# Performance work log

Hardware: AMD Instinct MI355X
Metric: run time of the kernel (lower is better)

## Reference

```python
import jax, jax.numpy as jnp
import numpy as np

N, D, E = 50000, 128, 600000
EPS = 1e-5  # LayerNorm eps (torch default)


def setup_inputs() -> dict:
    key = jax.random.key(0)
    ks = jax.random.split(key, 8)
    s = D ** -0.5
    return {
        "in_feat": jax.random.normal(ks[0], (N, D), dtype=jnp.float32),
        "edge_src": jax.random.randint(ks[1], (E,), 0, N),
        "edge_dst": jax.random.randint(ks[2], (E,), 0, N),
        "W1": jax.random.normal(ks[3], (D, D), dtype=jnp.float32) * s,
        "b1": jnp.zeros((D,), jnp.float32),
        "W2": jax.random.normal(ks[4], (D, D), dtype=jnp.float32) * s,
        "b2": jnp.zeros((D,), jnp.float32),
        "ln1_w": jnp.ones((D,), jnp.float32),
        "ln1_b": jnp.zeros((D,), jnp.float32),
        "ln2_w": jnp.ones((D,), jnp.float32),
        "ln2_b": jnp.zeros((D,), jnp.float32),
    }


def layer_norm(x, w, b):
    mu = jnp.mean(x, axis=-1, keepdims=True)
    var = jnp.var(x, axis=-1, keepdims=True)
    return (x - mu) * jax.lax.rsqrt(var + EPS) * w + b


def gcn_conv(x, W, b, src, dst, deg_inv_sqrt):
    # PyG GCNConv: linear transform, then D^-1/2 (A+I) D^-1/2 propagation, then bias
    h = x @ W  # [N, D]
    norm = deg_inv_sqrt[src] * deg_inv_sqrt[dst]  # [E]
    agg = jax.ops.segment_sum(h[src] * norm[:, None], dst, num_segments=N)
    agg = agg + (deg_inv_sqrt ** 2)[:, None] * h  # self-loop term handled analytically
    return agg + b


def reference(in_feat, W1, b1, W2, b2, ln1_w, ln1_b, ln2_w, ln2_b, edge_src, edge_dst):
    # degree with self-loops, computed on destination (PyG convention)
    deg = jax.ops.segment_sum(jnp.ones((E,), in_feat.dtype), edge_dst, num_segments=N) + 1.0
    dis = jax.lax.rsqrt(deg)
    h = gcn_conv(in_feat, W1, b1, edge_src, edge_dst, dis)
    ori = in_feat  # in_feats == h_feats -> residual uses original input
    ln_params = [(ln1_w, ln1_b), (ln2_w, ln2_b)]
    for i in range(2):  # prop_step - 1 iterations
        h = h + ori  # res=True, residual=1.0
        h = layer_norm(h, *ln_params[i])
        h = jax.nn.relu(h)  # dropout=0 -> identity
        h = gcn_conv(h, W2, b2, edge_src, edge_dst, dis)
    return h
```

## Files before the change

### kernel.cpp

```cpp
#include <hip/hip_runtime.h>
#include <hip/hip_bf16.h>

typedef unsigned short bf16_t;
typedef __attribute__((ext_vector_type(4))) float f32x4;
typedef __attribute__((ext_vector_type(8))) unsigned short us8;

#define CAP 64

__device__ __forceinline__ float bf2f(bf16_t u) {
  return __uint_as_float(((unsigned int)u) << 16);
}
__device__ __forceinline__ bf16_t f2bf(float f) {
  unsigned int u = __float_as_uint(f);
  return (bf16_t)((u + 0x7FFFu + ((u >> 16) & 1u)) >> 16);
}
__device__ __forceinline__ void acc2(float2& a, unsigned int d) {
  a.x += __uint_as_float(d << 16);
  a.y += __uint_as_float(d & 0xffff0000u);
}

__global__ void UnifiedGNN_56521769616171_kernel() {}


__global__ void gnn_zero(int* cnt, int n, bf16_t* Azrow, bf16_t* A2zrow,
                         const float* W1, const float* W2,
                         bf16_t* Wt1g, bf16_t* Wt2g) {
  int gid = blockIdx.x * 256 + threadIdx.x;
  if (blockIdx.x == 0 && threadIdx.x < 64) {
    ((unsigned int*)Azrow)[threadIdx.x] = 0u;
    ((unsigned int*)A2zrow)[threadIdx.x] = 0u;
  }
  if (gid < 4096) {
    const float* W = (gid < 2048) ? W1 : W2;
    bf16_t* dst = (gid < 2048) ? Wt1g : Wt2g;
    int j = gid & 2047;
    int c = j & 127;
    int kb = j >> 7;
    int k0 = kb << 3;
    us8 v;
#pragma unroll
    for (int q = 0; q < 8; q++) v[q] = f2bf(W[(size_t)(k0 + q) * 128 + c]);
    ((us8*)dst)[c * 16 + (kb ^ (c & 15))] = v;
  }
  if (gid < n) cnt[gid] = 0;
}

__global__ void gnn_fill(const int* src, const int* dst, int* cnt,
                         int* csr, int e, int n) {
  int i = blockIdx.x * 256 + threadIdx.x;
  if (i < e) {
    int d = dst[i];
    if (d >= 0 && d < n) {
      int pos = atomicAdd(&cnt[d], 1);
      if (pos < CAP) csr[(size_t)d * CAP + pos] = src[i];
    }
  }
}

__global__ __launch_bounds__(512) void gnn_gemm(const void* Xv,
    const bf16_t* Wg, const int* cnt, bf16_t* A, int n, int xfmt) {
  __shared__ __align__(16) bf16_t Wt[128 * 128];
  int tid = threadIdx.x;

  for (int j = tid; j < 2048; j += 512)
    ((us8*)Wt)[j] = ((const us8*)Wg)[j];
  __syncthreads();

  int lane = tid & 63;
  int wid = tid >> 6;
  int l15 = lane & 15;
  int lk = lane >> 4;
  const bf16_t* Xb = (const bf16_t*)Xv;
  const float* Xf = (const float*)Xv;

  int rowbase = blockIdx.x * 128 + wid * 16;
  int arow = rowbase + l15;
  int arc = arow < n ? arow : (n - 1);

  f32x4 acc[8];
#pragma unroll
  for (int c = 0; c < 8; c++) {
    acc[c][0] = 0.0f; acc[c][1] = 0.0f; acc[c][2] = 0.0f; acc[c][3] = 0.0f;
  }

#pragma unroll
  for (int ks = 0; ks < 4; ks++) {
    int kb = ks * 4 + lk;
    us8 ah, al;
    if (xfmt == 0) {
      float4 a0 = *(const float4*)(Xf + (size_t)arc * 128 + kb * 8);
      float4 a1 = *(const float4*)(Xf + (size_t)arc * 128 + kb * 8 + 4);
      ah[0] = f2bf(a0.x); al[0] = f2bf(a0.x - bf2f(ah[0]));
      ah[1] = f2bf(a0.y); al[1] = f2bf(a0.y - bf2f(ah[1]));
      ah[2] = f2bf(a0.z); al[2] = f2bf(a0.z - bf2f(ah[2]));
      ah[3] = f2bf(a0.w); al[3] = f2bf(a0.w - bf2f(ah[3]));
      ah[4] = f2bf(a1.x); al[4] = f2bf(a1.x - bf2f(ah[4]));
      ah[5] = f2bf(a1.y); al[5] = f2bf(a1.y - bf2f(ah[5]));
      ah[6] = f2bf(a1.z); al[6] = f2bf(a1.z - bf2f(ah[6]));
      ah[7] = f2bf(a1.w); al[7] = f2bf(a1.w - bf2f(ah[7]));
    } else {
      ah = *(const us8*)(Xb + (size_t)arc * 128 + kb * 8);
    }
#pragma unroll
    for (int c = 0; c < 8; c++) {
      int col = c * 16 + l15;
      us8 bf = *(const us8*)&Wt[col * 128 + ((kb ^ l15) << 3)];
      asm volatile("s_nop 2\n\tv_mfma_f32_16x16x32_bf16 %0, %1, %2, %0"
                   : "+v"(acc[c]) : "v"(ah), "v"(bf));
    }
    if (xfmt == 0) {
#pragma unroll
      for (int c = 0; c < 8; c++) {
        int col = c * 16 + l15;
        us8 bf = *(const us8*)&Wt[col * 128 + ((kb ^ l15) << 3)];
        asm volatile("s_nop 2\n\tv_mfma_f32_16x16x32_bf16 %0, %1, %2, %0"
                     : "+v"(acc[c]) : "v"(al), "v"(bf));
      }
    }
  }
  asm volatile("s_nop 7\n\ts_nop 7"
               : "+v"(acc[0]), "+v"(acc[1]), "+v"(acc[2]), "+v"(acc[3]),
                 "+v"(acc[4]), "+v"(acc[5]), "+v"(acc[6]), "+v"(acc[7]));

#pragma unroll
  for (int j = 0; j < 4; j++) {
    int row = rowbase + lk * 4 + j;
    if (row < n) {
      float dd = rsqrtf((float)cnt[row] + 1.0f);
#pragma unroll
      for (int c = 0; c < 8; c++) {
        A[(size_t)row * 128 + c * 16 + l15] = f2bf(acc[c][j] * dd);
      }
    }
  }
}

__global__ __launch_bounds__(512) void gnn_agg_gemm(const bf16_t* Ain,
    const int* cnt, const int* csr, const float* bias, const float* ori,
    const float* lnw, const float* lnb, const bf16_t* Wg,
    bf16_t* Aout, int n) {
  __shared__ __align__(16) bf16_t Wt[128 * 128];
  __shared__ __align__(16) bf16_t Bs[128 * 128];
  int tid = threadIdx.x;
  int lane = tid & 63;
  int wid = tid >> 6;
  int g = lane >> 4;
  int l16 = lane & 15;

  for (int j = tid; j < 2048; j += 512)
    ((us8*)Wt)[j] = ((const us8*)Wg)[j];

  const uint4* Av4 = (const uint4*)Ain;

  for (int rr = 0; rr < 4; rr++) {
    int rt = wid * 16 + rr * 4 + g;
    int row = blockIdx.x * 128 + rt;
    int rc = row < n ? row : (n - 1);
    int c = cnt[rc];
    int pc = (c + 15) & ~15;
    if (pc > CAP) pc = CAP;
    const int* crow = csr + (size_t)rc * CAP;

    float2 ac[4];
#pragma unroll
    for (int i = 0; i < 4; i++) ac[i] = make_float2(0.0f, 0.0f);

    for (int e = 0; e < pc; e += 16) {
      int raw = crow[e + l16];
      int sv = (e + l16 < c) ? raw : n;
#pragma unroll
      for (int half = 0; half < 2; half++) {
        uint4 va[8];
#pragma unroll
        for (int j = 0; j < 8; j++) {
          int s = __shfl(sv, (g << 4) + half * 8 + j);
          va[j] = Av4[(size_t)s * 16 + l16];
        }
#pragma unroll
        for (int j = 0; j < 8; j++) {
          acc2(ac[0], va[j].x);
          acc2(ac[1], va[j].y);
          acc2(ac[2], va[j].z);
          acc2(ac[3], va[j].w);
        }
      }
    }
    {
      uint4 sv4 = Av4[(size_t)rc * 16 + l16];
      acc2(ac[0], sv4.x);
      acc2(ac[1], sv4.y);
      acc2(ac[2], sv4.z);
      acc2(ac[3], sv4.w);
    }

    float dd = rsqrtf((float)c + 1.0f);
    float4 bb0 = *(const float4*)(bias + l16 * 8);
    float4 bb1 = *(const float4*)(bias + l16 * 8 + 4);
    float4 o0 = *(const float4*)(ori + (size_t)rc * 128 + l16 * 8);
    float4 o1 = *(const float4*)(ori + (size_t)rc * 128 + l16 * 8 + 4);
    float v[8];
    v[0] = dd * ac[0].x + bb0.x + o0.x; v[1] = dd * ac[0].y + bb0.y + o0.y;
    v[2] = dd * ac[1].x + bb0.z + o0.z; v[3] = dd * ac[1].y + bb0.w + o0.w;
    v[4] = dd * ac[2].x + bb1.x + o1.x; v[5] = dd * ac[2].y + bb1.y + o1.y;
    v[6] = dd * ac[3].x + bb1.z + o1.z; v[7] = dd * ac[3].y + bb1.w + o1.w;
    float s = 0.0f, sq = 0.0f;
#pragma unroll
    for (int i = 0; i < 8; i++) { s += v[i]; sq += v[i] * v[i]; }
    for (int off = 8; off >= 1; off >>= 1) {
      s += __shfl_xor(s, off);
      sq += __shfl_xor(sq, off);
    }
    float mu = s * (1.0f / 128.0f);
    float var = sq * (1.0f / 128.0f) - mu * mu;
    float inv = rsqrtf(var + 1e-5f);
    float4 w0 = *(const float4*)(lnw + l16 * 8);
    float4 w1 = *(const float4*)(lnw + l16 * 8 + 4);
    float4 c0 = *(const float4*)(lnb + l16 * 8);
    float4 c1 = *(const float4*)(lnb + l16 * 8 + 4);
    float wv[8] = {w0.x, w0.y, w0.z, w0.w, w1.x, w1.y, w1.z, w1.w};
    float cv[8] = {c0.x, c0.y, c0.z, c0.w, c1.x, c1.y, c1.z, c1.w};
    us8 o8;
#pragma unroll
    for (int i = 0; i < 8; i++) {
      float y = (v[i] - mu) * inv * wv[i] + cv[i];
      if (y < 0.0f) y = 0.0f;
      o8[i] = f2bf(y);
    }
    *(us8*)&Bs[rt * 128 + ((l16 ^ (rt & 15)) << 3)] = o8;
  }

  __syncthreads();

  int l15 = lane & 15;
  int lk = lane >> 4;
  int rowbase = blockIdx.x * 128 + wid * 16;
  int rt0 = wid * 16 + l15;

  f32x4 acc[8];
#pragma unroll
  for (int c = 0; c < 8; c++) {
    acc[c][0] = 0.0f; acc[c][1] = 0.0f; acc[c][2] = 0.0f; acc[c][3] = 0.0f;
  }

#pragma unroll
  for (int ks = 0; ks < 4; ks++) {
    int kb = ks * 4 + lk;
    us8 ah = *(const us8*)&Bs[rt0 * 128 + ((kb ^ l15) << 3)];
#pragma unroll
    for (int c = 0; c < 8; c++) {
      int col = c * 16 + l15;
      us8 bf = *(const us8*)&Wt[col * 128 + ((kb ^ l15) << 3)];
      asm volatile("s_nop 2\n\tv_mfma_f32_16x16x32_bf16 %0, %1, %2, %0"
                   : "+v"(acc[c]) : "v"(ah), "v"(bf));
    }
  }
  asm volatile("s_nop 7\n\ts_nop 7"
               : "+v"(acc[0]), "+v"(acc[1]), "+v"(acc[2]), "+v"(acc[3]),
                 "+v"(acc[4]), "+v"(acc[5]), "+v"(acc[6]), "+v"(acc[7]));

#pragma unroll
  for (int j = 0; j < 4; j++) {
    int row = rowbase + lk * 4 + j;
    if (row < n) {
      float dd = rsqrtf((float)cnt[row] + 1.0f);
#pragma unroll
      for (int c = 0; c < 8; c++) {
        Aout[(size_t)row * 128 + c * 16 + l15] = f2bf(acc[c][j] * dd);
      }
    }
  }
}

__global__ void gnn_aggln(const bf16_t* A,
    const int* cnt, const int* csr, const float* bias,
    float* Fout, int n) {
  int wid = threadIdx.x >> 6;
  int lane = threadIdx.x & 63;
  int g = lane >> 4;
  int l16 = lane & 15;
  int row = blockIdx.x * 16 + wid * 4 + g;
  bool active = row < n;
  int rc = active ? row : (n - 1);
  int c = cnt[rc];
  int pc = (c + 15) & ~15;
  if (pc > CAP) pc = CAP;
  const int* crow = csr + (size_t)rc * CAP;
  const uint4* Av4 = (const uint4*)A;

  float2 ac[4];
#pragma unroll
  for (int i = 0; i < 4; i++) ac[i] = make_float2(0.0f, 0.0f);

  for (int e = 0; e < pc; e += 16) {
    int raw = crow[e + l16];
    int sv = (e + l16 < c) ? raw : n;
#pragma unroll
    for (int half = 0; half < 2; half++) {
      uint4 va[8];
#pragma unroll
      for (int j = 0; j < 8; j++) {
        int s = __shfl(sv, (g << 4) + half * 8 + j);
        va[j] = Av4[(size_t)s * 16 + l16];
      }
#pragma unroll
      for (int j = 0; j < 8; j++) {
        acc2(ac[0], va[j].x);
        acc2(ac[1], va[j].y);
        acc2(ac[2], va[j].z);
        acc2(ac[3], va[j].w);
      }
    }
  }
  {
    uint4 sv4 = Av4[(size_t)rc * 16 + l16];
    acc2(ac[0], sv4.x);
    acc2(ac[1], sv4.y);
    acc2(ac[2], sv4.z);
    acc2(ac[3], sv4.w);
  }

  float dd = rsqrtf((float)c + 1.0f);
  float4 bb0 = *(const float4*)(bias + l16 * 8);
  float4 bb1 = *(const float4*)(bias + l16 * 8 + 4);
  if (active) {
    float4 f0 = make_float4(dd * ac[0].x + bb0.x, dd * ac[0].y + bb0.y,
                            dd * ac[1].x + bb0.z, dd * ac[1].y + bb0.w);
    float4 f1 = make_float4(dd * ac[2].x + bb1.x, dd * ac[2].y + bb1.y,
                            dd * ac[3].x + bb1.z, dd * ac[3].y + bb1.w);
    *(float4*)(Fout + (size_t)rc * 128 + l16 * 8) = f0;
    *(float4*)(Fout + (size_t)rc * 128 + l16 * 8 + 4) = f1;
  }
}


extern "C" void kernel_launch(void* const* d_in, const int* in_sizes, int n_in,
                              void* d_out, int out_size, void* d_ws, size_t ws_size,
                              hipStream_t stream) {
  UnifiedGNN_56521769616171_kernel<<<1, 64, 0, stream>>>();

  int nI = (n_in > 0 && n_in <= 16) ? n_in : 11;
  long best = -1;
  int iFeat = 0;
  for (int i = 0; i < nI; i++)
    if ((long)in_sizes[i] > best) { best = in_sizes[i]; iFeat = i; }
  int iW[2], iV[6], iE[2];
  int nW = 0, nV = 0, nE = 0;
  for (int i = 0; i < nI; i++) {
    if (i == iFeat) continue;
    int s = in_sizes[i];
    if (s == 128 * 128) { if (nW < 2) iW[nW++] = i; }
    else if (s == 128)  { if (nV < 6) iV[nV++] = i; }
    else                { if (nE < 2) iE[nE++] = i; }
  }
  int aFeat = 0, aEs = 1, aEd = 2, aW1 = 3, aB1 = 4, aW2 = 5, aB2 = 6,
      aL1w = 7, aL1b = 8, aL2w = 9, aL2b = 10;
  if (nW == 2 && nV == 6 && nE == 2) {
    aFeat = iFeat;
    aEs = iE[0]; aEd = iE[1];
    aW1 = iW[0]; aW2 = iW[1];
    aB1 = iV[0]; aB2 = iV[1];
    aL1w = iV[2]; aL1b = iV[3]; aL2w = iV[4]; aL2b = iV[5];
  }

  int N = 50000;
  int E = 600000;
  if (in_sizes[aFeat] > 0 && (in_sizes[aFeat] % 128) == 0) N = in_sizes[aFeat] / 128;
  if (in_sizes[aEs] > 0) E = in_sizes[aEs];

  const float* in_feat = (const float*)d_in[aFeat];
  const int*   esrc    = (const int*)d_in[aEs];
  const int*   edst    = (const int*)d_in[aEd];
  const float* W1      = (const float*)d_in[aW1];
  const float* b1      = (const float*)d_in[aB1];
  const float* W2      = (const float*)d_in[aW2];
  const float* b2      = (const float*)d_in[aB2];
  const float* ln1w    = (const float*)d_in[aL1w];
  const float* ln1b    = (const float*)d_in[aL1b];
  const float* ln2w    = (const float*)d_in[aL2w];
  const float* ln2b    = (const float*)d_in[aL2b];

  char* base = (char*)d_ws;
  size_t off = 0;
  int* cnt = (int*)(base + off);      off += ((size_t)N * 4 + 255) & ~(size_t)255;
  int* csr = (int*)(base + off);      off += ((size_t)N * CAP * 4 + 255) & ~(size_t)255;
  bf16_t* A = (bf16_t*)(base + off);  off += ((size_t)(N + 1) * 256 + 255) & ~(size_t)255;
  bf16_t* A2 = (bf16_t*)(base + off); off += ((size_t)(N + 1) * 256 + 255) & ~(size_t)255;
  bf16_t* Wt1g = (bf16_t*)(base + off); off += 32768;
  bf16_t* Wt2g = (bf16_t*)(base + off); off += 32768;

  int gZ = (N + 255) / 256;
  int gE = (E + 255) / 256;
  int nt128 = (N + 127) / 128;
  int agg_grid = (N + 15) / 16;

  gnn_zero<<<gZ, 256, 0, stream>>>(cnt, N, A + (size_t)N * 128,
                                   A2 + (size_t)N * 128, W1, W2, Wt1g, Wt2g);
  gnn_fill<<<gE, 256, 0, stream>>>(esrc, edst, cnt, csr, E, N);

  gnn_gemm<<<nt128, 512, 0, stream>>>(in_feat, Wt1g, cnt, A, N, 0);

  gnn_agg_gemm<<<nt128, 512, 0, stream>>>(A, cnt, csr, b1, in_feat,
                                          ln1w, ln1b, Wt2g, A2, N);

  gnn_agg_gemm<<<nt128, 512, 0, stream>>>(A2, cnt, csr, b2, in_feat,
                                          ln2w, ln2b, Wt2g, A, N);

  gnn_aggln<<<agg_grid, 256, 0, stream>>>(A, cnt, csr, b2, (float*)d_out, N);
}
```

Before: 248.4 us.

## Fuse all GNN stages into one cooperative persistent kernel with grid syncs

```diff
diff --git a/kernel.cpp b/kernel.cpp
--- a/kernel.cpp
+++ b/kernel.cpp
@@ -1,5 +1,8 @@
 #include <hip/hip_runtime.h>
 #include <hip/hip_bf16.h>
+#include <hip/hip_cooperative_groups.h>
+
+namespace cg = cooperative_groups;
 
 typedef unsigned short bf16_t;
 typedef __attribute__((ext_vector_type(4))) float f32x4;
@@ -20,6 +23,313 @@
 }
 
 __global__ void UnifiedGNN_56521769616171_kernel() {}
+
+__device__ __forceinline__ void gather_row(const uint4* Av4, const int* crow,
+    int c, int pc, int nzero, int g, int l16, float2* ac) {
+  for (int e = 0; e < pc; e += 16) {
+    int raw = crow[e + l16];
+    int sv = (e + l16 < c) ? raw : nzero;
+#pragma unroll
+    for (int half = 0; half < 2; half++) {
+      uint4 va[8];
+#pragma unroll
+      for (int j = 0; j < 8; j++) {
+        int s = __shfl(sv, (g << 4) + half * 8 + j);
+        va[j] = Av4[(size_t)s * 16 + l16];
+      }
+#pragma unroll
+      for (int j = 0; j < 8; j++) {
+        acc2(ac[0], va[j].x);
+        acc2(ac[1], va[j].y);
+        acc2(ac[2], va[j].z);
+        acc2(ac[3], va[j].w);
+      }
+    }
+  }
+}
+
+__device__ __forceinline__ void agg_gemm_tile(const bf16_t* Ain, bf16_t* Aout,
+    const int* cnt, const int* csr, const float* bias, const float* ori,
+    const float* lnw, const float* lnb, bf16_t* Wt, bf16_t* Bs,
+    int n, int nt, int bid, int nblk) {
+  int tid = threadIdx.x;
+  int lane = tid & 63;
+  int wid = tid >> 6;
+  int g = lane >> 4;
+  int l16 = lane & 15;
+  const uint4* Av4 = (const uint4*)Ain;
+
+  for (int t = bid; t < nt; t += nblk) {
+    for (int rr = 0; rr < 4; rr++) {
+      int rt = wid * 16 + rr * 4 + g;
+      int row = t * 128 + rt;
+      int rc = row < n ? row : (n - 1);
+      int c = cnt[rc];
+      int pc = (c + 15) & ~15;
+      if (pc > CAP) pc = CAP;
+      float2 ac[4];
+#pragma unroll
+      for (int i = 0; i < 4; i++) ac[i] = make_float2(0.0f, 0.0f);
+      gather_row(Av4, csr + (size_t)rc * CAP, c, pc, n, g, l16, ac);
+      {
+        uint4 sv4 = Av4[(size_t)rc * 16 + l16];
+        acc2(ac[0], sv4.x);
+        acc2(ac[1], sv4.y);
+        acc2(ac[2], sv4.z);
+        acc2(ac[3], sv4.w);
+      }
+      float dd = rsqrtf((float)c + 1.0f);
+      float4 bb0 = *(const float4*)(bias + l16 * 8);
+      float4 bb1 = *(const float4*)(bias + l16 * 8 + 4);
+      float4 o0 = *(const float4*)(ori + (size_t)rc * 128 + l16 * 8);
+      float4 o1 = *(const float4*)(ori + (size_t)rc * 128 + l16 * 8 + 4);
+      float v[8];
+      v[0] = dd * ac[0].x + bb0.x + o0.x; v[1] = dd * ac[0].y + bb0.y + o0.y;
+      v[2] = dd * ac[1].x + bb0.z + o0.z; v[3] = dd * ac[1].y + bb0.w + o0.w;
+      v[4] = dd * ac[2].x + bb1.x + o1.x; v[5] = dd * ac[2].y + bb1.y + o1.y;
+      v[6] = dd * ac[3].x + bb1.z + o1.z; v[7] = dd * ac[3].y + bb1.w + o1.w;
+      float s = 0.0f, sq = 0.0f;
+#pragma unroll
+      for (int i = 0; i < 8; i++) { s += v[i]; sq += v[i] * v[i]; }
+      for (int off = 8; off >= 1; off >>= 1) {
+        s += __shfl_xor(s, off);
+        sq += __shfl_xor(sq, off);
+      }
+      float mu = s * (1.0f / 128.0f);
+      float var = sq * (1.0f / 128.0f) - mu * mu;
+      float inv = rsqrtf(var + 1e-5f);
+      float4 w0 = *(const float4*)(lnw + l16 * 8);
+      float4 w1 = *(const float4*)(lnw + l16 * 8 + 4);
+      float4 c0 = *(const float4*)(lnb + l16 * 8);
+      float4 c1 = *(const float4*)(lnb + l16 * 8 + 4);
+      float wv[8] = {w0.x, w0.y, w0.z, w0.w, w1.x, w1.y, w1.z, w1.w};
+      float cv[8] = {c0.x, c0.y, c0.z, c0.w, c1.x, c1.y, c1.z, c1.w};
+      us8 o8;
+#pragma unroll
+      for (int i = 0; i < 8; i++) {
+        float y = (v[i] - mu) * inv * wv[i] + cv[i];
+        if (y < 0.0f) y = 0.0f;
+        o8[i] = f2bf(y);
+      }
+      *(us8*)&Bs[rt * 128 + ((l16 ^ (rt & 15)) << 3)] = o8;
+    }
+
+    __syncthreads();
+
+    int l15 = lane & 15;
+    int lk = lane >> 4;
+    int rowbase = t * 128 + wid * 16;
+    int rt0 = wid * 16 + l15;
+
+    f32x4 acc[8];
+#pragma unroll
+    for (int cc = 0; cc < 8; cc++) {
+      acc[cc][0] = 0.0f; acc[cc][1] = 0.0f; acc[cc][2] = 0.0f; acc[cc][3] = 0.0f;
+    }
+#pragma unroll
+    for (int ks = 0; ks < 4; ks++) {
+      int kb = ks * 4 + lk;
+      us8 ah = *(const us8*)&Bs[rt0 * 128 + ((kb ^ l15) << 3)];
+#pragma unroll
+      for (int cc = 0; cc < 8; cc++) {
+        int col = cc * 16 + l15;
+        us8 bf = *(const us8*)&Wt[col * 128 + ((kb ^ l15) << 3)];
+        asm volatile("s_nop 2\n\tv_mfma_f32_16x16x32_bf16 %0, %1, %2, %0"
+                     : "+v"(acc[cc]) : "v"(ah), "v"(bf));
+      }
+    }
+    asm volatile("s_nop 7\n\ts_nop 7"
+                 : "+v"(acc[0]), "+v"(acc[1]), "+v"(acc[2]), "+v"(acc[3]),
+                   "+v"(acc[4]), "+v"(acc[5]), "+v"(acc[6]), "+v"(acc[7]));
+#pragma unroll
+    for (int j = 0; j < 4; j++) {
+      int row = rowbase + lk * 4 + j;
+      if (row < n) {
+        float dd = rsqrtf((float)cnt[row] + 1.0f);
+#pragma unroll
+        for (int cc = 0; cc < 8; cc++) {
+          Aout[(size_t)row * 128 + cc * 16 + l15] = f2bf(acc[cc][j] * dd);
+        }
+      }
+    }
+    __syncthreads();
+  }
+}
+
+struct MegaArgs {
+  const float* in_feat; const int* esrc; const int* edst;
+  const float* W1; const float* W2; const float* b1; const float* b2;
+  const float* ln1w; const float* ln1b; const float* ln2w; const float* ln2b;
+  int* cnt; int* csr; bf16_t* A; bf16_t* A2; bf16_t* Wt1g; bf16_t* Wt2g;
+  float* out; int n; int e; int nt;
+};
+
+__global__ __launch_bounds__(512, 4) void gnn_mega(MegaArgs a) {
+  cg::grid_group grid = cg::this_grid();
+  __shared__ __align__(16) bf16_t Wt[128 * 128];
+  __shared__ __align__(16) bf16_t Bs[128 * 128];
+  int tid = threadIdx.x;
+  int bid = blockIdx.x;
+  int nblk = gridDim.x;
+  long gid = (long)bid * 512 + tid;
+  long gstride = (long)nblk * 512;
+
+  for (long i = gid; i < a.n; i += gstride) a.cnt[i] = 0;
+  if (gid < 64) {
+    ((unsigned int*)(a.A + (size_t)a.n * 128))[gid] = 0u;
+  } else if (gid < 128) {
+    ((unsigned int*)(a.A2 + (size_t)a.n * 128))[gid - 64] = 0u;
+  }
+  if (gid < 4096) {
+    const float* W = (gid < 2048) ? a.W1 : a.W2;
+    bf16_t* dst = (gid < 2048) ? a.Wt1g : a.Wt2g;
+    int j = (int)gid & 2047;
+    int c = j & 127;
+    int kb = j >> 7;
+    int k0 = kb << 3;
+    us8 v;
+#pragma unroll
+    for (int q = 0; q < 8; q++) v[q] = f2bf(W[(size_t)(k0 + q) * 128 + c]);
+    ((us8*)dst)[c * 16 + (kb ^ (c & 15))] = v;
+  }
+  grid.sync();
+
+  for (long i = gid; i < a.e; i += 3 * gstride) {
+    long i1 = i + gstride, i2 = i + 2 * gstride;
+    int d0 = a.edst[i], s0 = a.esrc[i];
+    int d1 = -1, s1 = 0, d2 = -1, s2 = 0;
+    if (i1 < a.e) { d1 = a.edst[i1]; s1 = a.esrc[i1]; }
+    if (i2 < a.e) { d2 = a.edst[i2]; s2 = a.esrc[i2]; }
+    if (d0 >= 0 && d0 < a.n) {
+      int p = atomicAdd(&a.cnt[d0], 1);
+      if (p < CAP) a.csr[(size_t)d0 * CAP + p] = s0;
+    }
+    if (d1 >= 0 && d1 < a.n) {
+      int p = atomicAdd(&a.cnt[d1], 1);
+      if (p < CAP) a.csr[(size_t)d1 * CAP + p] = s1;
+    }
+    if (d2 >= 0 && d2 < a.n) {
+      int p = atomicAdd(&a.cnt[d2], 1);
+      if (p < CAP) a.csr[(size_t)d2 * CAP + p] = s2;
+    }
+  }
+  grid.sync();
+
+  {
+    for (int j = tid; j < 2048; j += 512)
+      ((us8*)Wt)[j] = ((const us8*)a.Wt1g)[j];
+    __syncthreads();
+    int lane = tid & 63;
+    int wid = tid >> 6;
+    int l15 = lane & 15;
+    int lk = lane >> 4;
+    for (int t = bid; t < a.nt; t += nblk) {
+      int rowbase = t * 128 + wid * 16;
+      int arow = rowbase + l15;
+      int arc = arow < a.n ? arow : (a.n - 1);
+      f32x4 acc[8];
+#pragma unroll
+      for (int cc = 0; cc < 8; cc++) {
+        acc[cc][0] = 0.0f; acc[cc][1] = 0.0f; acc[cc][2] = 0.0f; acc[cc][3] = 0.0f;
+      }
+#pragma unroll
+      for (int ks = 0; ks < 4; ks++) {
+        int kb = ks * 4 + lk;
+        us8 ah, al;
+        float4 a0 = *(const float4*)(a.in_feat + (size_t)arc * 128 + kb * 8);
+        float4 a1 = *(const float4*)(a.in_feat + (size_t)arc * 128 + kb * 8 + 4);
+        ah[0] = f2bf(a0.x); al[0] = f2bf(a0.x - bf2f(ah[0]));
+        ah[1] = f2bf(a0.y); al[1] = f2bf(a0.y - bf2f(ah[1]));
+        ah[2] = f2bf(a0.z); al[2] = f2bf(a0.z - bf2f(ah[2]));
+        ah[3] = f2bf(a0.w); al[3] = f2bf(a0.w - bf2f(ah[3]));
+        ah[4] = f2bf(a1.x); al[4] = f2bf(a1.x - bf2f(ah[4]));
+        ah[5] = f2bf(a1.y); al[5] = f2bf(a1.y - bf2f(ah[5]));
+        ah[6] = f2bf(a1.z); al[6] = f2bf(a1.z - bf2f(ah[6]));
+        ah[7] = f2bf(a1.w); al[7] = f2bf(a1.w - bf2f(ah[7]));
+#pragma unroll
+        for (int cc = 0; cc < 8; cc++) {
+          int col = cc * 16 + l15;
+          us8 bf = *(const us8*)&Wt[col * 128 + ((kb ^ l15) << 3)];
+          asm volatile("s_nop 2\n\tv_mfma_f32_16x16x32_bf16 %0, %1, %2, %0"
+                       : "+v"(acc[cc]) : "v"(ah), "v"(bf));
+        }
+#pragma unroll
+        for (int cc = 0; cc < 8; cc++) {
+          int col = cc * 16 + l15;
+          us8 bf = *(const us8*)&Wt[col * 128 + ((kb ^ l15) << 3)];
+          asm volatile("s_nop 2\n\tv_mfma_f32_16x16x32_bf16 %0, %1, %2, %0"
+                       : "+v"(acc[cc]) : "v"(al), "v"(bf));
+        }
+      }
+      asm volatile("s_nop 7\n\ts_nop 7"
+                   : "+v"(acc[0]), "+v"(acc[1]), "+v"(acc[2]), "+v"(acc[3]),
+                     "+v"(acc[4]), "+v"(acc[5]), "+v"(acc[6]), "+v"(acc[7]));
+#pragma unroll
+      for (int j = 0; j < 4; j++) {
+        int row = rowbase + lk * 4 + j;
+        if (row < a.n) {
+          float dd = rsqrtf((float)a.cnt[row] + 1.0f);
+#pragma unroll
+          for (int cc = 0; cc < 8; cc++) {
+            a.A[(size_t)row * 128 + cc * 16 + l15] = f2bf(acc[cc][j] * dd);
+          }
+        }
+      }
+    }
+  }
+  grid.sync();
+
+  for (int j = tid; j < 2048; j += 512)
+    ((us8*)Wt)[j] = ((const us8*)a.Wt2g)[j];
+  agg_gemm_tile(a.A, a.A2, a.cnt, a.csr, a.b1, a.in_feat, a.ln1w, a.ln1b,
+                Wt, Bs, a.n, a.nt, bid, nblk);
+  grid.sync();
+
+  agg_gemm_tile(a.A2, a.A, a.cnt, a.csr, a.b2, a.in_feat, a.ln2w, a.ln2b,
+                Wt, Bs, a.n, a.nt, bid, nblk);
+  grid.sync();
+
+  {
+    int lane = tid & 63;
+    int g = lane >> 4;
+    int l16 = lane & 15;
+    int gg = tid >> 4;
+    const uint4* Av4 = (const uint4*)a.A;
+    for (int t = bid; t < a.nt; t += nblk) {
+#pragma unroll
+      for (int pass = 0; pass < 4; pass++) {
+        int row = t * 128 + pass * 32 + gg;
+        bool active = row < a.n;
+        int rc = active ? row : (a.n - 1);
+        int c = a.cnt[rc];
+        int pc = (c + 15) & ~15;
+        if (pc > CAP) pc = CAP;
+        float2 ac[4];
+#pragma unroll
+        for (int i = 0; i < 4; i++) ac[i] = make_float2(0.0f, 0.0f);
+        gather_row(Av4, a.csr + (size_t)rc * CAP, c, pc, a.n, g, l16, ac);
+        {
+          uint4 sv4 = Av4[(size_t)rc * 16 + l16];
+          acc2(ac[0], sv4.x);
+          acc2(ac[1], sv4.y);
+          acc2(ac[2], sv4.z);
+          acc2(ac[3], sv4.w);
+        }
+        float dd = rsqrtf((float)c + 1.0f);
+        float4 bb0 = *(const float4*)(a.b2 + l16 * 8);
+        float4 bb1 = *(const float4*)(a.b2 + l16 * 8 + 4);
+        if (active) {
+          float4 f0 = make_float4(dd * ac[0].x + bb0.x, dd * ac[0].y + bb0.y,
+                                  dd * ac[1].x + bb0.z, dd * ac[1].y + bb0.w);
+          float4 f1 = make_float4(dd * ac[2].x + bb1.x, dd * ac[2].y + bb1.y,
+                                  dd * ac[3].x + bb1.z, dd * ac[3].y + bb1.w);
+          *(float4*)(a.out + (size_t)rc * 128 + l16 * 8) = f0;
+          *(float4*)(a.out + (size_t)rc * 128 + l16 * 8 + 4) = f1;
+        }
+      }
+    }
+  }
+}
 
 
 __global__ void gnn_zero(int* cnt, int n, bf16_t* Azrow, bf16_t* A2zrow,
@@ -61,28 +371,23 @@
     const bf16_t* Wg, const int* cnt, bf16_t* A, int n, int xfmt) {
   __shared__ __align__(16) bf16_t Wt[128 * 128];
   int tid = threadIdx.x;
-
   for (int j = tid; j < 2048; j += 512)
     ((us8*)Wt)[j] = ((const us8*)Wg)[j];
   __syncthreads();
-
   int lane = tid & 63;
   int wid = tid >> 6;
   int l15 = lane & 15;
   int lk = lane >> 4;
   const bf16_t* Xb = (const bf16_t*)Xv;
   const float* Xf = (const float*)Xv;
-
   int rowbase = blockIdx.x * 128 + wid * 16;
   int arow = rowbase + l15;
   int arc = arow < n ? arow : (n - 1);
-
   f32x4 acc[8];
 #pragma unroll
   for (int c = 0; c < 8; c++) {
     acc[c][0] = 0.0f; acc[c][1] = 0.0f; acc[c][2] = 0.0f; acc[c][3] = 0.0f;
   }
-
 #pragma unroll
   for (int ks = 0; ks < 4; ks++) {
     int kb = ks * 4 + lk;
@@ -121,7 +426,6 @@
   asm volatile("s_nop 7\n\ts_nop 7"
                : "+v"(acc[0]), "+v"(acc[1]), "+v"(acc[2]), "+v"(acc[3]),
                  "+v"(acc[4]), "+v"(acc[5]), "+v"(acc[6]), "+v"(acc[7]));
-
 #pragma unroll
   for (int j = 0; j < 4; j++) {
     int row = rowbase + lk * 4 + j;
@@ -142,133 +446,10 @@
   __shared__ __align__(16) bf16_t Wt[128 * 128];
   __shared__ __align__(16) bf16_t Bs[128 * 128];
   int tid = threadIdx.x;
-  int lane = tid & 63;
-  int wid = tid >> 6;
-  int g = lane >> 4;
-  int l16 = lane & 15;
-
   for (int j = tid; j < 2048; j += 512)
     ((us8*)Wt)[j] = ((const us8*)Wg)[j];
-
-  const uint4* Av4 = (const uint4*)Ain;
-
-  for (int rr = 0; rr < 4; rr++) {
-    int rt = wid * 16 + rr * 4 + g;
-    int row = blockIdx.x * 128 + rt;
-    int rc = row < n ? row : (n - 1);
-    int c = cnt[rc];
-    int pc = (c + 15) & ~15;
-    if (pc > CAP) pc = CAP;
-    const int* crow = csr + (size_t)rc * CAP;
-
-    float2 ac[4];
-#pragma unroll
-    for (int i = 0; i < 4; i++) ac[i] = make_float2(0.0f, 0.0f);
-
-    for (int e = 0; e < pc; e += 16) {
-      int raw = crow[e + l16];
-      int sv = (e + l16 < c) ? raw : n;
-#pragma unroll
-      for (int half = 0; half < 2; half++) {
-        uint4 va[8];
-#pragma unroll
-        for (int j = 0; j < 8; j++) {
-          int s = __shfl(sv, (g << 4) + half * 8 + j);
-          va[j] = Av4[(size_t)s * 16 + l16];
-        }
-#pragma unroll
-        for (int j = 0; j < 8; j++) {
-          acc2(ac[0], va[j].x);
-          acc2(ac[1], va[j].y);
-          acc2(ac[2], va[j].z);
-          acc2(ac[3], va[j].w);
-        }
-      }
-    }
-    {
-      uint4 sv4 = Av4[(size_t)rc * 16 + l16];
-      acc2(ac[0], sv4.x);
-      acc2(ac[1], sv4.y);
-      acc2(ac[2], sv4.z);
-      acc2(ac[3], sv4.w);
-    }
-
-    float dd = rsqrtf((float)c + 1.0f);
-    float4 bb0 = *(const float4*)(bias + l16 * 8);
-    float4 bb1 = *(const float4*)(bias + l16 * 8 + 4);
-    float4 o0 = *(const float4*)(ori + (size_t)rc * 128 + l16 * 8);
-    float4 o1 = *(const float4*)(ori + (size_t)rc * 128 + l16 * 8 + 4);
-    float v[8];
-    v[0] = dd * ac[0].x + bb0.x + o0.x; v[1] = dd * ac[0].y + bb0.y + o0.y;
-    v[2] = dd * ac[1].x + bb0.z + o0.z; v[3] = dd * ac[1].y + bb0.w + o0.w;
-    v[4] = dd * ac[2].x + bb1.x + o1.x; v[5] = dd * ac[2].y + bb1.y + o1.y;
-    v[6] = dd * ac[3].x + bb1.z + o1.z; v[7] = dd * ac[3].y + bb1.w + o1.w;
-    float s = 0.0f, sq = 0.0f;
-#pragma unroll
-    for (int i = 0; i < 8; i++) { s += v[i]; sq += v[i] * v[i]; }
-    for (int off = 8; off >= 1; off >>= 1) {
-      s += __shfl_xor(s, off);
-      sq += __shfl_xor(sq, off);
-    }
-    float mu = s * (1.0f / 128.0f);
-    float var = sq * (1.0f / 128.0f) - mu * mu;
-    float inv = rsqrtf(var + 1e-5f);
-    float4 w0 = *(const float4*)(lnw + l16 * 8);
-    float4 w1 = *(const float4*)(lnw + l16 * 8 + 4);
-    float4 c0 = *(const float4*)(lnb + l16 * 8);
-    float4 c1 = *(const float4*)(lnb + l16 * 8 + 4);
-    float wv[8] = {w0.x, w0.y, w0.z, w0.w, w1.x, w1.y, w1.z, w1.w};
-    float cv[8] = {c0.x, c0.y, c0.z, c0.w, c1.x, c1.y, c1.z, c1.w};
-    us8 o8;
-#pragma unroll
-    for (int i = 0; i < 8; i++) {
-      float y = (v[i] - mu) * inv * wv[i] + cv[i];
-      if (y < 0.0f) y = 0.0f;
-      o8[i] = f2bf(y);
-    }
-    *(us8*)&Bs[rt * 128 + ((l16 ^ (rt & 15)) << 3)] = o8;
-  }
-
-  __syncthreads();
-
-  int l15 = lane & 15;
-  int lk = lane >> 4;
-  int rowbase = blockIdx.x * 128 + wid * 16;
-  int rt0 = wid * 16 + l15;
-
-  f32x4 acc[8];
-#pragma unroll
-  for (int c = 0; c < 8; c++) {
-    acc[c][0] = 0.0f; acc[c][1] = 0.0f; acc[c][2] = 0.0f; acc[c][3] = 0.0f;
-  }
-
-#pragma unroll
-  for (int ks = 0; ks < 4; ks++) {
-    int kb = ks * 4 + lk;
-    us8 ah = *(const us8*)&Bs[rt0 * 128 + ((kb ^ l15) << 3)];
-#pragma unroll
-    for (int c = 0; c < 8; c++) {
-      int col = c * 16 + l15;
-      us8 bf = *(const us8*)&Wt[col * 128 + ((kb ^ l15) << 3)];
-      asm volatile("s_nop 2\n\tv_mfma_f32_16x16x32_bf16 %0, %1, %2, %0"
-                   : "+v"(acc[c]) : "v"(ah), "v"(bf));
-    }
-  }
-  asm volatile("s_nop 7\n\ts_nop 7"
-               : "+v"(acc[0]), "+v"(acc[1]), "+v"(acc[2]), "+v"(acc[3]),
-                 "+v"(acc[4]), "+v"(acc[5]), "+v"(acc[6]), "+v"(acc[7]));
-
-#pragma unroll
-  for (int j = 0; j < 4; j++) {
-    int row = rowbase + lk * 4 + j;
-    if (row < n) {
-      float dd = rsqrtf((float)cnt[row] + 1.0f);
-#pragma unroll
-      for (int c = 0; c < 8; c++) {
-        Aout[(size_t)row * 128 + c * 16 + l15] = f2bf(acc[c][j] * dd);
-      }
-    }
-  }
+  agg_gemm_tile(Ain, Aout, cnt, csr, bias, ori, lnw, lnb, Wt, Bs, n,
+                gridDim.x, blockIdx.x, gridDim.x);
 }
 
 __global__ void gnn_aggln(const bf16_t* A,
@@ -284,33 +465,11 @@
   int c = cnt[rc];
   int pc = (c + 15) & ~15;
   if (pc > CAP) pc = CAP;
-  const int* crow = csr + (size_t)rc * CAP;
   const uint4* Av4 = (const uint4*)A;
-
   float2 ac[4];
 #pragma unroll
   for (int i = 0; i < 4; i++) ac[i] = make_float2(0.0f, 0.0f);
-
-  for (int e = 0; e < pc; e += 16) {
-    int raw = crow[e + l16];
-    int sv = (e + l16 < c) ? raw : n;
-#pragma unroll
-    for (int half = 0; half < 2; half++) {
-      uint4 va[8];
-#pragma unroll
-      for (int j = 0; j < 8; j++) {
-        int s = __shfl(sv, (g << 4) + half * 8 + j);
-        va[j] = Av4[(size_t)s * 16 + l16];
-      }
-#pragma unroll
-      for (int j = 0; j < 8; j++) {
-        acc2(ac[0], va[j].x);
-        acc2(ac[1], va[j].y);
-        acc2(ac[2], va[j].z);
-        acc2(ac[3], va[j].w);
-      }
-    }
-  }
+  gather_row(Av4, csr + (size_t)rc * CAP, c, pc, n, g, l16, ac);
   {
     uint4 sv4 = Av4[(size_t)rc * 16 + l16];
     acc2(ac[0], sv4.x);
@@ -318,7 +477,6 @@
     acc2(ac[2], sv4.z);
     acc2(ac[3], sv4.w);
   }
-
   float dd = rsqrtf((float)c + 1.0f);
   float4 bb0 = *(const float4*)(bias + l16 * 8);
   float4 bb1 = *(const float4*)(bias + l16 * 8 + 4);
@@ -388,22 +546,31 @@
   bf16_t* Wt1g = (bf16_t*)(base + off); off += 32768;
   bf16_t* Wt2g = (bf16_t*)(base + off); off += 32768;
 
-  int gZ = (N + 255) / 256;
-  int gE = (E + 255) / 256;
-  int nt128 = (N + 127) / 128;
-  int agg_grid = (N + 15) / 16;
-
-  gnn_zero<<<gZ, 256, 0, stream>>>(cnt, N, A + (size_t)N * 128,
-                                   A2 + (size_t)N * 128, W1, W2, Wt1g, Wt2g);
-  gnn_fill<<<gE, 256, 0, stream>>>(esrc, edst, cnt, csr, E, N);
-
-  gnn_gemm<<<nt128, 512, 0, stream>>>(in_feat, Wt1g, cnt, A, N, 0);
-
-  gnn_agg_gemm<<<nt128, 512, 0, stream>>>(A, cnt, csr, b1, in_feat,
-                                          ln1w, ln1b, Wt2g, A2, N);
-
-  gnn_agg_gemm<<<nt128, 512, 0, stream>>>(A2, cnt, csr, b2, in_feat,
-                                          ln2w, ln2b, Wt2g, A, N);
-
-  gnn_aggln<<<agg_grid, 256, 0, stream>>>(A, cnt, csr, b2, (float*)d_out, N);
-}
+  int nt = (N + 127) / 128;
+  int nblk = nt < 512 ? nt : 512;
+
+  MegaArgs ma;
+  ma.in_feat = in_feat; ma.esrc = esrc; ma.edst = edst;
+  ma.W1 = W1; ma.W2 = W2; ma.b1 = b1; ma.b2 = b2;
+  ma.ln1w = ln1w; ma.ln1b = ln1b; ma.ln2w = ln2w; ma.ln2b = ln2b;
+  ma.cnt = cnt; ma.csr = csr; ma.A = A; ma.A2 = A2;
+  ma.Wt1g = Wt1g; ma.Wt2g = Wt2g; ma.out = (float*)d_out;
+  ma.n = N; ma.e = E; ma.nt = nt;
+  void* params[] = {&ma};
+  hipError_t rc = hipLaunchCooperativeKernel((void*)gnn_mega, dim3(nblk),
+                                             dim3(512), params, 0, stream);
+  if (rc != hipSuccess) {
+    int gZ = (N + 255) / 256;
+    int gE = (E + 255) / 256;
+    int agg_grid = (N + 15) / 16;
+    gnn_zero<<<gZ, 256, 0, stream>>>(cnt, N, A + (size_t)N * 128,
+                                     A2 + (size_t)N * 128, W1, W2, Wt1g, Wt2g);
+    gnn_fill<<<gE, 256, 0, stream>>>(esrc, edst, cnt, csr, E, N);
+    gnn_gemm<<<nt, 512, 0, stream>>>(in_feat, Wt1g, cnt, A, N, 0);
+    gnn_agg_gemm<<<nt, 512, 0, stream>>>(A, cnt, csr, b1, in_feat,
+                                         ln1w, ln1b, Wt2g, A2, N);
+    gnn_agg_gemm<<<nt, 512, 0, stream>>>(A2, cnt, csr, b2, in_feat,
+                                         ln2w, ln2b, Wt2g, A, N);
+    gnn_aggln<<<agg_grid, 256, 0, stream>>>(A, cnt, csr, b2, (float*)d_out, N);
+  }
+}
```

New measurement: 526.3 us. +111.9%, slower.
